# Performance work log

Measured on AMD Instinct MI355X. Metric: run time of the kernel, lower is better.

## Reference

```python
import jax, jax.numpy as jnp
import numpy as np

D_KQ = 1024

def setup_inputs() -> dict:
    key = jax.random.key(0)
    k1, k2, k3, k4, k5 = jax.random.split(key, 5)
    x = jax.random.normal(k1, (4, 2048, 1024), dtype=jnp.float32)
    attention_mask = jax.random.randint(k2, (2048, 2048), 0, 2) == 1
    q_weights = jax.random.normal(k3, (1024, 1024), dtype=jnp.float32)
    k_weights = jax.random.normal(k4, (1024, 1024), dtype=jnp.float32)
    v_weights = jax.random.normal(k5, (1024, 1024), dtype=jnp.float32)
    return {"x": x, "attention_mask": attention_mask,
            "q_weights": q_weights, "k_weights": k_weights, "v_weights": v_weights}

def reference(x, attention_mask, q_weights, k_weights, v_weights):
    # projections: [B,S,d_in] @ [d_in,d] -> [B,S,d]
    query = x @ q_weights
    key = x @ k_weights
    value = x @ v_weights
    # scores: [B,S,S]
    attn_scores = jnp.einsum('bqd,bkd->bqk', query, key)
    masked = jnp.where(attention_mask, -jnp.inf, attn_scores)
    attn_weights = jax.nn.softmax(masked / jnp.sqrt(jnp.float32(D_KQ)), axis=-1)
    return attn_weights @ value
```

## Files before the change

kernel.cpp:

```cpp
#include <hip/hip_runtime.h>
#include <math.h>

static constexpr int BATCH = 4;
static constexpr int SEQ   = 2048;
static constexpr int DIM   = 1024;

typedef __attribute__((ext_vector_type(8))) short     bf16x8;
typedef __attribute__((ext_vector_type(4))) float     f32x4;

__device__ __forceinline__ unsigned short f2b(float v) {
    unsigned int u = __float_as_uint(v);
    u = u + 0x7fffu + ((u >> 16) & 1u);
    return (unsigned short)(u >> 16);
}
__device__ __forceinline__ float b2f(unsigned short h) {
    return __uint_as_float(((unsigned int)h) << 16);
}

__global__ __launch_bounds__(256) void prep_kernel(
    const float* __restrict__ X, const float* __restrict__ Wq,
    const float* __restrict__ Wk, const float* __restrict__ Wv,
    const int* __restrict__ mask,
    unsigned short* __restrict__ Xhi, unsigned short* __restrict__ Xlo,
    unsigned short* __restrict__ Whi, unsigned short* __restrict__ Wlo,
    unsigned short* __restrict__ WvT, unsigned long long* __restrict__ Mb)
{
    __shared__ float t[32][33];
    const int blk = blockIdx.x;
    const int tid = threadIdx.x;

    if (blk < 8192) {
        const int i = blk * 256 + tid;
        const float4 v = ((const float4*)X)[i];
        ushort4 h, l;
        h.x = f2b(v.x); l.x = f2b(v.x - b2f(h.x));
        h.y = f2b(v.y); l.y = f2b(v.y - b2f(h.y));
        h.z = f2b(v.z); l.z = f2b(v.z - b2f(h.z));
        h.w = f2b(v.w); l.w = f2b(v.w - b2f(h.w));
        ((ushort4*)Xhi)[i] = h;
        ((ushort4*)Xlo)[i] = l;
    } else if (blk < 10240) {
        const int lcl = blk - 8192;
        const int z = lcl >> 10;
        const float* __restrict__ W = z ? Wk : Wq;
        const int i = (lcl & 1023) * 256 + tid;
        const int o = z * (DIM * DIM / 4) + i;
        const float4 v = ((const float4*)W)[i];
        ushort4 h, l;
        h.x = f2b(v.x); l.x = f2b(v.x - b2f(h.x));
        h.y = f2b(v.y); l.y = f2b(v.y - b2f(h.y));
        h.z = f2b(v.z); l.z = f2b(v.z - b2f(h.z));
        h.w = f2b(v.w); l.w = f2b(v.w - b2f(h.w));
        ((ushort4*)Whi)[o] = h;
        ((ushort4*)Wlo)[o] = l;
    } else if (blk < 11264) {
        const int lcl = blk - 10240;
        const int n0 = (lcl & 31) * 32, k0 = (lcl >> 5) * 32;
        const int tx = tid & 31, ty = tid >> 5;
#pragma unroll
        for (int i = 0; i < 4; ++i)
            t[ty + i * 8][tx] = Wv[(size_t)(k0 + ty + i * 8) * DIM + (n0 + tx)];
        __syncthreads();
#pragma unroll
        for (int i = 0; i < 4; ++i)
            WvT[(size_t)(n0 + ty + i * 8) * DIM + (k0 + tx)] = f2b(t[tx][ty + i * 8]);
    } else {
        const int row  = blk - 11264;
        const int lane = tid & 63, w = tid >> 6;
#pragma unroll
        for (int c = w; c < SEQ / 64; c += 4) {
            const int v = mask[(size_t)row * SEQ + c * 64 + lane];
            const unsigned long long bits = __ballot(v != 0);
            if (lane == 0) Mb[(size_t)row * (SEQ / 64) + c] = bits;
        }
    }
}

__device__ __forceinline__ void stage_async(
    const unsigned short* __restrict__ g, int gstride, int row0, int k0,
    unsigned short* lds, int tid)
{
    const int w = tid >> 6, lane = tid & 63;
    const int c = (lane & 3) ^ ((lane >> 4) & 3);
#pragma unroll
    for (int h = 0; h < 2; ++h) {
        const int row = 32 * w + 16 * h + (lane >> 2);
        const unsigned short* src = g + (size_t)(row0 + row) * gstride + k0 + 8 * c;
        unsigned short* dst = lds + (32 * w + 16 * h) * 32;
        __builtin_amdgcn_global_load_lds(
            (const __attribute__((address_space(1))) void*)src,
            (__attribute__((address_space(3))) void*)dst, 16, 0, 0);
    }
}

__device__ __forceinline__ void stage128(
    const unsigned short* __restrict__ g, int gstride, int row0, int k0,
    unsigned short* lds, int tid)
{
    const int w = tid >> 6, lane = tid & 63;
    const int c = (lane & 3) ^ ((lane >> 4) & 3);
    const int row = 16 * w + (lane >> 2);
    const unsigned short* src = g + (size_t)(row0 + row) * gstride + k0 + 8 * c;
    unsigned short* dst = lds + (16 * w) * 32;
    __builtin_amdgcn_global_load_lds(
        (const __attribute__((address_space(1))) void*)src,
        (__attribute__((address_space(3))) void*)dst, 16, 0, 0);
}

__device__ __forceinline__ bf16x8 fragr(const unsigned short* lds, int row, int qsw)
{
    return *(const bf16x8*)(lds + row * 32 + qsw * 8);
}

__global__ __launch_bounds__(256) void m_gemm_kernel(
    const unsigned short* __restrict__ Whi, const unsigned short* __restrict__ Wlo,
    float* __restrict__ Mtp)
{
    __shared__ unsigned short Ah[128 * 32], Al[128 * 32];
    __shared__ unsigned short Bh[128 * 32], Bl[128 * 32];

    const int tid = threadIdx.x;
    const int w = tid >> 6, lane = tid & 63;
    const int wm = (w >> 1) * 64, wn = (w & 1) * 64;
    const int m0 = blockIdx.y * 128, n0 = blockIdx.x * 128;
    const int z = blockIdx.z;

    const unsigned short* __restrict__ Ahg = Whi + (size_t)DIM * DIM;
    const unsigned short* __restrict__ Alg = Wlo + (size_t)DIM * DIM;
    const unsigned short* __restrict__ Bhg = Whi;
    const unsigned short* __restrict__ Blg = Wlo;
    float* __restrict__ Cp = Mtp + (size_t)z * DIM * DIM;

    f32x4 acc[4][4];
#pragma unroll
    for (int i = 0; i < 4; ++i)
#pragma unroll
        for (int j = 0; j < 4; ++j) acc[i][j] = (f32x4){0.f, 0.f, 0.f, 0.f};

    const int fr = lane & 15, quad = lane >> 4;
    const int qsw = quad ^ ((fr >> 2) & 3);

    for (int k0 = z * 256; k0 < z * 256 + 256; k0 += 32) {
        stage_async(Ahg, DIM, m0, k0, Ah, tid);
        stage_async(Alg, DIM, m0, k0, Al, tid);
        stage_async(Bhg, DIM, n0, k0, Bh, tid);
        stage_async(Blg, DIM, n0, k0, Bl, tid);
        __syncthreads();

        bf16x8 ah[4], al[4];
#pragma unroll
        for (int mt = 0; mt < 4; ++mt) {
            ah[mt] = fragr(Ah, wm + mt * 16 + fr, qsw);
            al[mt] = fragr(Al, wm + mt * 16 + fr, qsw);
        }
#pragma unroll
        for (int nt = 0; nt < 4; ++nt) {
            const bf16x8 bh = fragr(Bh, wn + nt * 16 + fr, qsw);
            const bf16x8 bl = fragr(Bl, wn + nt * 16 + fr, qsw);
#pragma unroll
            for (int mt = 0; mt < 4; ++mt) {
                acc[mt][nt] = __builtin_amdgcn_mfma_f32_16x16x32_bf16(ah[mt], bh, acc[mt][nt], 0, 0, 0);
                acc[mt][nt] = __builtin_amdgcn_mfma_f32_16x16x32_bf16(ah[mt], bl, acc[mt][nt], 0, 0, 0);
                acc[mt][nt] = __builtin_amdgcn_mfma_f32_16x16x32_bf16(al[mt], bh, acc[mt][nt], 0, 0, 0);
            }
        }
        __syncthreads();
    }

    const int col = lane & 15, rq = lane >> 4;
#pragma unroll
    for (int mt = 0; mt < 4; ++mt)
#pragma unroll
        for (int nt = 0; nt < 4; ++nt)
#pragma unroll
            for (int e = 0; e < 4; ++e) {
                const int m = m0 + wm + mt * 16 + rq * 4 + e;
                const int n = n0 + wn + nt * 16 + col;
                Cp[(size_t)m * DIM + n] = acc[mt][nt][e];
            }
}

__global__ __launch_bounds__(256) void m_reduce_kernel(
    const float* __restrict__ Mtp, unsigned short* __restrict__ Mthi,
    unsigned short* __restrict__ Mtlo)
{
    const int i = blockIdx.x * 256 + threadIdx.x;
    const size_t q = (size_t)DIM * DIM / 4;
    const float4 a = ((const float4*)Mtp)[i];
    const float4 b = ((const float4*)Mtp)[i + q];
    const float4 c = ((const float4*)Mtp)[i + 2 * q];
    const float4 d = ((const float4*)Mtp)[i + 3 * q];
    const float4 v = make_float4(a.x + b.x + c.x + d.x, a.y + b.y + c.y + d.y,
                                 a.z + b.z + c.z + d.z, a.w + b.w + c.w + d.w);
    ushort4 h, l;
    h.x = f2b(v.x); l.x = f2b(v.x - b2f(h.x));
    h.y = f2b(v.y); l.y = f2b(v.y - b2f(h.y));
    h.z = f2b(v.z); l.z = f2b(v.z - b2f(h.z));
    h.w = f2b(v.w); l.w = f2b(v.w - b2f(h.w));
    ((ushort4*)Mthi)[i] = h;
    ((ushort4*)Mtlo)[i] = l;
}

__global__ __launch_bounds__(512, 2) void yv_gemm_kernel(
    const unsigned short* __restrict__ Xhi, const unsigned short* __restrict__ Xlo,
    const unsigned short* __restrict__ Mthi, const unsigned short* __restrict__ Mtlo,
    const unsigned short* __restrict__ WvT,
    unsigned short* __restrict__ Yhi, unsigned short* __restrict__ Ylo,
    unsigned short* __restrict__ Vt)
{
    extern __shared__ unsigned short smem[];

    const int tid = threadIdx.x;
    const int w = tid >> 6, lane = tid & 63;
    const int wm = (w >> 1) * 64, wn = (w & 1) * 64;

    const int flat = blockIdx.x + (blockIdx.y << 3);
    const int xcd = flat & 7, s = flat >> 3;
    const int m0 = (xcd + ((s >> 3) << 3)) * 256;
    const int n0 = (s & 7) * 128;

    f32x4 accY[4][4], accV[4][4];
#pragma unroll
    for (int i = 0; i < 4; ++i)
#pragma unroll
        for (int j = 0; j < 4; ++j) {
            accY[i][j] = (f32x4){0.f, 0.f, 0.f, 0.f};
            accV[i][j] = (f32x4){0.f, 0.f, 0.f, 0.f};
        }

    const int fr = lane & 15, quad = lane >> 4;
    const int qsw = quad ^ ((fr >> 2) & 3);

    stage_async(Xhi, DIM, m0, 0, smem + 0,     tid);
    stage128(Mthi, DIM, n0, 0, smem + 16384, tid);
    stage128(Mtlo, DIM, n0, 0, smem + 20480, tid);
    stage_async(Xlo, DIM, m0, 0, smem + 8192,  tid);
    stage128(WvT,  DIM, n0, 0, smem + 24576, tid);

    bf16x8 ah[4], al[4], bh[4], bl[4], bv[4];

    for (int it = 0; it < DIM / 32 - 1; ++it) {
        const int cur = (it & 1) * 28672;
        const int nxt = 28672 - cur;
        const int k1 = it * 32 + 32;

        stage_async(Xhi, DIM, m0, k1, smem + nxt, tid);
        asm volatile("s_waitcnt vmcnt(6)" ::: "memory");
        __builtin_amdgcn_s_barrier();
#pragma unroll
        for (int mt = 0; mt < 4; ++mt)
            ah[mt] = fragr(smem + cur, wm + mt * 16 + fr, qsw);
#pragma unroll
        for (int nt = 0; nt < 4; ++nt)
            bh[nt] = fragr(smem + cur + 16384, wn + nt * 16 + fr, qsw);
        __builtin_amdgcn_s_setprio(1);
#pragma unroll
        for (int nt = 0; nt < 4; ++nt)
#pragma unroll
            for (int mt = 0; mt < 4; ++mt)
                accY[mt][nt] = __builtin_amdgcn_mfma_f32_16x16x32_bf16(ah[mt], bh[nt], accY[mt][nt], 0, 0, 0);
        __builtin_amdgcn_s_setprio(0);

        stage128(Mthi, DIM, n0, k1, smem + nxt + 16384, tid);
        stage128(Mtlo, DIM, n0, k1, smem + nxt + 20480, tid);
        asm volatile("s_waitcnt vmcnt(7)" ::: "memory");
        __builtin_amdgcn_s_barrier();
#pragma unroll
        for (int nt = 0; nt < 4; ++nt)
            bl[nt] = fragr(smem + cur + 20480, wn + nt * 16 + fr, qsw);
        __builtin_amdgcn_s_setprio(1);
#pragma unroll
        for (int nt = 0; nt < 4; ++nt)
#pragma unroll
            for (int mt = 0; mt < 4; ++mt)
                accY[mt][nt] = __builtin_amdgcn_mfma_f32_16x16x32_bf16(ah[mt], bl[nt], accY[mt][nt], 0, 0, 0);
        __builtin_amdgcn_s_setprio(0);

        stage_async(Xlo, DIM, m0, k1, smem + nxt + 8192, tid);
        asm volatile("s_waitcnt vmcnt(6)" ::: "memory");
        __builtin_amdgcn_s_barrier();
#pragma unroll
        for (int nt = 0; nt < 4; ++nt)
            bv[nt] = fragr(smem + cur + 24576, wn + nt * 16 + fr, qsw);
        __builtin_amdgcn_s_setprio(1);
#pragma unroll
        for (int nt = 0; nt < 4; ++nt)
#pragma unroll
            for (int mt = 0; mt < 4; ++mt)
                accV[mt][nt] = __builtin_amdgcn_mfma_f32_16x16x32_bf16(ah[mt], bv[nt], accV[mt][nt], 0, 0, 0);
        __builtin_amdgcn_s_setprio(0);

        stage128(WvT, DIM, n0, k1, smem + nxt + 24576, tid);
        asm volatile("s_waitcnt vmcnt(8)" ::: "memory");
        __builtin_amdgcn_s_barrier();
#pragma unroll
        for (int mt = 0; mt < 4; ++mt)
            al[mt] = fragr(smem + cur + 8192, wm + mt * 16 + fr, qsw);
        __builtin_amdgcn_s_setprio(1);
#pragma unroll
        for (int nt = 0; nt < 4; ++nt)
#pragma unroll
            for (int mt = 0; mt < 4; ++mt)
                accY[mt][nt] = __builtin_amdgcn_mfma_f32_16x16x32_bf16(al[mt], bh[nt], accY[mt][nt], 0, 0, 0);
        __builtin_amdgcn_s_setprio(0);
    }

    {
        const int cur = 28672;

        asm volatile("s_waitcnt vmcnt(4)" ::: "memory");
        __builtin_amdgcn_s_barrier();
#pragma unroll
        for (int mt = 0; mt < 4; ++mt)
            ah[mt] = fragr(smem + cur, wm + mt * 16 + fr, qsw);
#pragma unroll
        for (int nt = 0; nt < 4; ++nt)
            bh[nt] = fragr(smem + cur + 16384, wn + nt * 16 + fr, qsw);
        __builtin_amdgcn_s_setprio(1);
#pragma unroll
        for (int nt = 0; nt < 4; ++nt)
#pragma unroll
            for (int mt = 0; mt < 4; ++mt)
                accY[mt][nt] = __builtin_amdgcn_mfma_f32_16x16x32_bf16(ah[mt], bh[nt], accY[mt][nt], 0, 0, 0);
        __builtin_amdgcn_s_setprio(0);

        asm volatile("s_waitcnt vmcnt(3)" ::: "memory");
        __builtin_amdgcn_s_barrier();
#pragma unroll
        for (int nt = 0; nt < 4; ++nt)
            bl[nt] = fragr(smem + cur + 20480, wn + nt * 16 + fr, qsw);
        __builtin_amdgcn_s_setprio(1);
#pragma unroll
        for (int nt = 0; nt < 4; ++nt)
#pragma unroll
            for (int mt = 0; mt < 4; ++mt)
                accY[mt][nt] = __builtin_amdgcn_mfma_f32_16x16x32_bf16(ah[mt], bl[nt], accY[mt][nt], 0, 0, 0);
        __builtin_amdgcn_s_setprio(0);

        asm volatile("s_waitcnt vmcnt(0)" ::: "memory");
        __builtin_amdgcn_s_barrier();
#pragma unroll
        for (int nt = 0; nt < 4; ++nt)
            bv[nt] = fragr(smem + cur + 24576, wn + nt * 16 + fr, qsw);
        __builtin_amdgcn_s_setprio(1);
#pragma unroll
        for (int nt = 0; nt < 4; ++nt)
#pragma unroll
            for (int mt = 0; mt < 4; ++mt)
                accV[mt][nt] = __builtin_amdgcn_mfma_f32_16x16x32_bf16(ah[mt], bv[nt], accV[mt][nt], 0, 0, 0);
        __builtin_amdgcn_s_setprio(0);

#pragma unroll
        for (int mt = 0; mt < 4; ++mt)
            al[mt] = fragr(smem + cur + 8192, wm + mt * 16 + fr, qsw);
        __builtin_amdgcn_s_setprio(1);
#pragma unroll
        for (int nt = 0; nt < 4; ++nt)
#pragma unroll
            for (int mt = 0; mt < 4; ++mt)
                accY[mt][nt] = __builtin_amdgcn_mfma_f32_16x16x32_bf16(al[mt], bh[nt], accY[mt][nt], 0, 0, 0);
        __builtin_amdgcn_s_setprio(0);
    }

    const int col = lane & 15, rq = lane >> 4;
#pragma unroll
    for (int mt = 0; mt < 4; ++mt)
#pragma unroll
        for (int nt = 0; nt < 4; ++nt)
#pragma unroll
            for (int e = 0; e < 4; ++e) {
                const int m = m0 + wm + mt * 16 + rq * 4 + e;
                const int n = n0 + wn + nt * 16 + col;
                const float v = accY[mt][nt][e];
                const unsigned short h = f2b(v);
                Yhi[(size_t)m * DIM + n] = h;
                Ylo[(size_t)m * DIM + n] = f2b(v - b2f(h));
            }
#pragma unroll
    for (int mt = 0; mt < 4; ++mt)
#pragma unroll
        for (int nt = 0; nt < 4; ++nt) {
            const int m = m0 + wm + mt * 16 + rq * 4;
            const int bb = m >> 11, sr = m & (SEQ - 1);
            const int n = n0 + wn + nt * 16 + col;
            ushort4 pk;
            pk.x = f2b(accV[mt][nt][0]);
            pk.y = f2b(accV[mt][nt][1]);
            pk.z = f2b(accV[mt][nt][2]);
            pk.w = f2b(accV[mt][nt][3]);
            *(ushort4*)(Vt + (size_t)bb * DIM * SEQ + (size_t)n * SEQ + sr) = pk;
        }
}

__global__ __launch_bounds__(512, 2) void s_gemm256_kernel(
    const unsigned short* __restrict__ Yhi, const unsigned short* __restrict__ Ylo,
    const unsigned short* __restrict__ Xhi, const unsigned short* __restrict__ Xlo,
    const unsigned long long* __restrict__ Mb, float* __restrict__ Sc)
{
    extern __shared__ unsigned short smem[];

    const int tid = threadIdx.x;
    const int w = tid >> 6, lane = tid & 63;
    const int wm = (w >> 2) * 128, wn = (w & 3) * 64;

    const int flat = blockIdx.x + (blockIdx.y << 3) + (blockIdx.z << 6);
    const int lid  = ((flat & 7) << 5) | (flat >> 3);
    const int m0 = ((lid >> 3) & 7) * 256, n0 = (lid & 7) * 256;
    const int b  = lid >> 6;

    const unsigned short* __restrict__ Ahg = Yhi + (size_t)b * SEQ * DIM;
    const unsigned short* __restrict__ Alg = Ylo + (size_t)b * SEQ * DIM;
    const unsigned short* __restrict__ Bhg = Xhi + (size_t)b * SEQ * DIM;
    const unsigned short* __restrict__ Blg = Xlo + (size_t)b * SEQ * DIM;
    float* __restrict__ Sb = Sc + (size_t)b * SEQ * SEQ;

    f32x4 acc[8][4];
#pragma unroll
    for (int i = 0; i < 8; ++i)
#pragma unroll
        for (int j = 0; j < 4; ++j) acc[i][j] = (f32x4){0.f, 0.f, 0.f, 0.f};

    const int fr = lane & 15, quad = lane >> 4;
    const int qsw = quad ^ ((fr >> 2) & 3);

    stage_async(Ahg, DIM, m0, 0, smem + 0,     tid);
    stage_async(Bhg, DIM, n0, 0, smem + 16384, tid);
    stage_async(Blg, DIM, n0, 0, smem + 24576, tid);
    stage_async(Alg, DIM, m0, 0, smem + 8192,  tid);

    for (int it = 0; it < DIM / 32 - 1; ++it) {
        const int cur = (it & 1) * 32768;
        const int nxt = cur ^ 32768;
        const unsigned short* Ah = smem + cur;
        const unsigned short* Al = smem + cur + 8192;
        const unsigned short* Bh = smem + cur + 16384;
        const unsigned short* Bl = smem + cur + 24576;
        const int k1 = it * 32 + 32;

        bf16x8 ah[8], al[8], bh[4], bl[4];

        stage_async(Ahg, DIM, m0, k1, smem + nxt, tid);
        asm volatile("s_waitcnt vmcnt(6)" ::: "memory");
        __builtin_amdgcn_s_barrier();
#pragma unroll
        for (int mt = 0; mt < 4; ++mt)
            ah[mt] = fragr(Ah, wm + mt * 16 + fr, qsw);
#pragma unroll
        for (int nt = 0; nt < 4; ++nt)
            bh[nt] = fragr(Bh, wn + nt * 16 + fr, qsw);
        __builtin_amdgcn_s_setprio(1);
#pragma unroll
        for (int nt = 0; nt < 4; ++nt)
#pragma unroll
            for (int mt = 0; mt < 4; ++mt)
                acc[mt][nt] = __builtin_amdgcn_mfma_f32_16x16x32_bf16(ah[mt], bh[nt], acc[mt][nt], 0, 0, 0);
        __builtin_amdgcn_s_setprio(0);

        stage_async(Bhg, DIM, n0, k1, smem + nxt + 16384, tid);
#pragma unroll
        for (int mt = 4; mt < 8; ++mt)
            ah[mt] = fragr(Ah, wm + mt * 16 + fr, qsw);
        __builtin_amdgcn_s_setprio(1);
#pragma unroll
        for (int nt = 0; nt < 4; ++nt)
#pragma unroll
            for (int mt = 4; mt < 8; ++mt)
                acc[mt][nt] = __builtin_amdgcn_mfma_f32_16x16x32_bf16(ah[mt], bh[nt], acc[mt][nt], 0, 0, 0);
        __builtin_amdgcn_s_setprio(0);

        stage_async(Blg, DIM, n0, k1, smem + nxt + 24576, tid);
        asm volatile("s_waitcnt vmcnt(8)" ::: "memory");
        __builtin_amdgcn_s_barrier();
#pragma unroll
        for (int nt = 0; nt < 4; ++nt)
            bl[nt] = fragr(Bl, wn + nt * 16 + fr, qsw);
        __builtin_amdgcn_s_setprio(1);
#pragma unroll
        for (int nt = 0; nt < 4; ++nt)
#pragma unroll
            for (int mt = 0; mt < 4; ++mt)
                acc[mt][nt] = __builtin_amdgcn_mfma_f32_16x16x32_bf16(ah[mt], bl[nt], acc[mt][nt], 0, 0, 0);
        __builtin_amdgcn_s_setprio(0);

        __builtin_amdgcn_s_setprio(1);
#pragma unroll
        for (int nt = 0; nt < 4; ++nt)
#pragma unroll
            for (int mt = 4; mt < 8; ++mt)
                acc[mt][nt] = __builtin_amdgcn_mfma_f32_16x16x32_bf16(ah[mt], bl[nt], acc[mt][nt], 0, 0, 0);
        __builtin_amdgcn_s_setprio(0);

        stage_async(Alg, DIM, m0, k1, smem + nxt + 8192, tid);
        asm volatile("s_waitcnt vmcnt(8)" ::: "memory");
        __builtin_amdgcn_s_barrier();
#pragma unroll
        for (int mt = 0; mt < 4; ++mt)
            al[mt] = fragr(Al, wm + mt * 16 + fr, qsw);
        __builtin_amdgcn_s_setprio(1);
#pragma unroll
        for (int nt = 0; nt < 4; ++nt)
#pragma unroll
            for (int mt = 0; mt < 4; ++mt)
                acc[mt][nt] = __builtin_amdgcn_mfma_f32_16x16x32_bf16(al[mt], bh[nt], acc[mt][nt], 0, 0, 0);
        __builtin_amdgcn_s_setprio(0);

#pragma unroll
        for (int mt = 4; mt < 8; ++mt)
            al[mt] = fragr(Al, wm + mt * 16 + fr, qsw);
        __builtin_amdgcn_s_setprio(1);
#pragma unroll
        for (int nt = 0; nt < 4; ++nt)
#pragma unroll
            for (int mt = 4; mt < 8; ++mt)
                acc[mt][nt] = __builtin_amdgcn_mfma_f32_16x16x32_bf16(al[mt], bh[nt], acc[mt][nt], 0, 0, 0);
        __builtin_amdgcn_s_setprio(0);
    }

    {
        const unsigned short* Ah = smem + 32768;
        const unsigned short* Al = smem + 32768 + 8192;
        const unsigned short* Bh = smem + 32768 + 16384;
        const unsigned short* Bl = smem + 32768 + 24576;

        bf16x8 ah[8], al[8], bh[4], bl[4];

        asm volatile("s_waitcnt vmcnt(4)" ::: "memory");
        __builtin_amdgcn_s_barrier();
#pragma unroll
        for (int mt = 0; mt < 8; ++mt)
            ah[mt] = fragr(Ah, wm + mt * 16 + fr, qsw);
#pragma unroll
        for (int nt = 0; nt < 4; ++nt)
            bh[nt] = fragr(Bh, wn + nt * 16 + fr, qsw);
        __builtin_amdgcn_s_setprio(1);
#pragma unroll
        for (int nt = 0; nt < 4; ++nt)
#pragma unroll
            for (int mt = 0; mt < 8; ++mt)
                acc[mt][nt] = __builtin_amdgcn_mfma_f32_16x16x32_bf16(ah[mt], bh[nt], acc[mt][nt], 0, 0, 0);
        __builtin_amdgcn_s_setprio(0);

        asm volatile("s_waitcnt vmcnt(2)" ::: "memory");
        __builtin_amdgcn_s_barrier();
#pragma unroll
        for (int nt = 0; nt < 4; ++nt)
            bl[nt] = fragr(Bl, wn + nt * 16 + fr, qsw);
        __builtin_amdgcn_s_setprio(1);
#pragma unroll
        for (int nt = 0; nt < 4; ++nt)
#pragma unroll
            for (int mt = 0; mt < 8; ++mt)
                acc[mt][nt] = __builtin_amdgcn_mfma_f32_16x16x32_bf16(ah[mt], bl[nt], acc[mt][nt], 0, 0, 0);
        __builtin_amdgcn_s_setprio(0);

        asm volatile("s_waitcnt vmcnt(0)" ::: "memory");
        __builtin_amdgcn_s_barrier();
#pragma unroll
        for (int mt = 0; mt < 8; ++mt)
            al[mt] = fragr(Al, wm + mt * 16 + fr, qsw);
        __builtin_amdgcn_s_setprio(1);
#pragma unroll
        for (int nt = 0; nt < 4; ++nt)
#pragma unroll
            for (int mt = 0; mt < 8; ++mt)
                acc[mt][nt] = __builtin_amdgcn_mfma_f32_16x16x32_bf16(al[mt], bh[nt], acc[mt][nt], 0, 0, 0);
        __builtin_amdgcn_s_setprio(0);
    }

    const int col = lane & 15, rq = lane >> 4;
    const int wword = (n0 + wn) >> 6;
#pragma unroll
    for (int mt = 0; mt < 8; ++mt)
#pragma unroll
        for (int e = 0; e < 4; ++e) {
            const int m = m0 + wm + mt * 16 + rq * 4 + e;
            const unsigned long long word = Mb[(size_t)m * (SEQ / 64) + wword];
#pragma unroll
            for (int nt = 0; nt < 4; ++nt) {
                const int n = n0 + wn + nt * 16 + col;
                const float v = acc[mt][nt][e] * 0.03125f;
                const bool msk = (word >> (nt * 16 + col)) & 1ull;
                Sb[(size_t)m * SEQ + n] = msk ? -INFINITY : v;
            }
        }
}

__global__ __launch_bounds__(256) void softmax_kernel(float* __restrict__ Sc)
{
    const int r = blockIdx.x;
    float* __restrict__ row = Sc + (size_t)r * SEQ;

    const int tid  = threadIdx.x;
    const int lane = tid & 63;
    const int wid  = tid >> 6;

    const float4 v0 = ((const float4*)row)[2 * tid];
    const float4 v1 = ((const float4*)row)[2 * tid + 1];
    float x[8] = {v0.x, v0.y, v0.z, v0.w, v1.x, v1.y, v1.z, v1.w};

    float mx = -INFINITY;
#pragma unroll
    for (int j = 0; j < 8; ++j) mx = fmaxf(mx, x[j]);
    __shared__ float redm[4];
#pragma unroll
    for (int off = 32; off > 0; off >>= 1)
        mx = fmaxf(mx, __shfl_down(mx, off, 64));
    if (lane == 0) redm[wid] = mx;
    __syncthreads();
    mx = fmaxf(fmaxf(redm[0], redm[1]), fmaxf(redm[2], redm[3]));

    float sum = 0.f;
#pragma unroll
    for (int j = 0; j < 8; ++j) {
        const float e = __expf(x[j] - mx);
        x[j] = e;
        sum += e;
    }
    __shared__ float reds[4];
#pragma unroll
    for (int off = 32; off > 0; off >>= 1)
        sum += __shfl_down(sum, off, 64);
    if (lane == 0) reds[wid] = sum;
    __syncthreads();
    sum = (reds[0] + reds[1]) + (reds[2] + reds[3]);

    const float inv = 1.0f / sum;
    unsigned short* __restrict__ prow = (unsigned short*)row;
    bf16x8 pk;
#pragma unroll
    for (int j = 0; j < 8; ++j)
        pk[j] = (short)f2b(x[j] * inv);
    *(bf16x8*)(prow + 8 * tid) = pk;
}

__global__ __launch_bounds__(256) void pv_mfma_kernel(
    const unsigned short* __restrict__ P, const unsigned short* __restrict__ Vt,
    float* __restrict__ O)
{
    __shared__ unsigned short As[2][128 * 32], Bs[2][128 * 32];

    const int tid = threadIdx.x;
    const int w = tid >> 6, lane = tid & 63;
    const int wm = (w >> 1) * 64, wn = (w & 1) * 64;

    const int flat = blockIdx.x + (blockIdx.y << 3) + (blockIdx.z << 7);
    const int lid  = ((flat & 7) << 6) | (flat >> 3);
    const int m0 = ((lid >> 3) & 15) * 128, n0 = (lid & 7) * 128;
    const int b  = lid >> 7;

    const unsigned short* __restrict__ Ag = P + (size_t)b * SEQ * (2 * SEQ);
    const unsigned short* __restrict__ Bg = Vt + (size_t)b * DIM * SEQ;
    float* __restrict__ Ob = O + (size_t)b * SEQ * DIM;

    f32x4 acc[4][4];
#pragma unroll
    for (int i = 0; i < 4; ++i)
#pragma unroll
        for (int j = 0; j < 4; ++j) acc[i][j] = (f32x4){0.f, 0.f, 0.f, 0.f};

    const int fr = lane & 15, quad = lane >> 4;
    const int qsw = quad ^ ((fr >> 2) & 3);

    stage_async(Ag, 2 * SEQ, m0, 0, As[0], tid);
    stage_async(Bg, SEQ,     n0, 0, Bs[0], tid);

    for (int it = 0; it < SEQ / 32 - 1; ++it) {
        const int cur = it & 1, nxt = cur ^ 1;
        const int k1 = it * 32 + 32;

        stage_async(Ag, 2 * SEQ, m0, k1, As[nxt], tid);
        stage_async(Bg, SEQ,     n0, k1, Bs[nxt], tid);
        asm volatile("s_waitcnt vmcnt(4)" ::: "memory");
        __builtin_amdgcn_s_barrier();

        bf16x8 af[4];
#pragma unroll
        for (int mt = 0; mt < 4; ++mt)
            af[mt] = fragr(As[cur], wm + mt * 16 + fr, qsw);
        __builtin_amdgcn_s_setprio(1);
#pragma unroll
        for (int nt = 0; nt < 4; ++nt) {
            const bf16x8 bfg = fragr(Bs[cur], wn + nt * 16 + fr, qsw);
#pragma unroll
            for (int mt = 0; mt < 4; ++mt)
                acc[mt][nt] = __builtin_amdgcn_mfma_f32_16x16x32_bf16(af[mt], bfg, acc[mt][nt], 0, 0, 0);
        }
        __builtin_amdgcn_s_setprio(0);
        __builtin_amdgcn_s_barrier();
    }

    {
        asm volatile("s_waitcnt vmcnt(0)" ::: "memory");
        __builtin_amdgcn_s_barrier();
        bf16x8 af[4];
#pragma unroll
        for (int mt = 0; mt < 4; ++mt)
            af[mt] = fragr(As[1], wm + mt * 16 + fr, qsw);
        __builtin_amdgcn_s_setprio(1);
#pragma unroll
        for (int nt = 0; nt < 4; ++nt) {
            const bf16x8 bfg = fragr(Bs[1], wn + nt * 16 + fr, qsw);
#pragma unroll
            for (int mt = 0; mt < 4; ++mt)
                acc[mt][nt] = __builtin_amdgcn_mfma_f32_16x16x32_bf16(af[mt], bfg, acc[mt][nt], 0, 0, 0);
        }
        __builtin_amdgcn_s_setprio(0);
    }

    const int col = lane & 15, rq = lane >> 4;
#pragma unroll
    for (int mt = 0; mt < 4; ++mt)
#pragma unroll
        for (int nt = 0; nt < 4; ++nt)
#pragma unroll
            for (int e = 0; e < 4; ++e) {
                const int m = m0 + wm + mt * 16 + rq * 4 + e;
                const int n = n0 + wn + nt * 16 + col;
                Ob[(size_t)m * DIM + n] = acc[mt][nt][e];
            }
}

extern "C" void kernel_launch(void* const* d_in, const int* in_sizes, int n_in,
                              void* d_out, int out_size, void* d_ws, size_t ws_size,
                              hipStream_t stream)
{
    const float* x    = (const float*)d_in[0];
    const int*   mask = (const int*)d_in[1];
    const float* wq   = (const float*)d_in[2];
    const float* wk   = (const float*)d_in[3];
    const float* wv   = (const float*)d_in[4];
    float* out = (float*)d_out;

    const size_t NQ = (size_t)BATCH * SEQ * DIM;
    const size_t NM = (size_t)DIM * DIM;
    unsigned short* Xhi  = (unsigned short*)d_ws;
    unsigned short* Xlo  = Xhi + NQ;
    unsigned short* Yhi  = Xlo + NQ;
    unsigned short* Ylo  = Yhi + NQ;
    unsigned short* Vt   = Ylo + NQ;
    unsigned short* Mthi = Vt + NQ;
    unsigned short* Mtlo = Mthi + NM;
    float* Sc = (float*)(Mtlo + NM);
    unsigned long long* Mb = (unsigned long long*)(Sc + (size_t)BATCH * SEQ * SEQ);

    unsigned short* Whi = (unsigned short*)Sc;
    unsigned short* Wlo = Whi + 2 * NM;
    unsigned short* WvT = Wlo + 2 * NM;
    float* Mtp = (float*)(WvT + NM);

    static bool lds_attr_set = false;
    if (!lds_attr_set) {
        (void)hipFuncSetAttribute((const void*)s_gemm256_kernel,
                                  hipFuncAttributeMaxDynamicSharedMemorySize,
                                  131072);
        (void)hipFuncSetAttribute((const void*)yv_gemm_kernel,
                                  hipFuncAttributeMaxDynamicSharedMemorySize,
                                  114688);
        lds_attr_set = true;
    }

    prep_kernel<<<dim3(13312), 256, 0, stream>>>(
        x, wq, wk, wv, mask, Xhi, Xlo, Whi, Wlo, WvT, Mb);
    m_gemm_kernel<<<dim3(8, 8, 4), 256, 0, stream>>>(Whi, Wlo, Mtp);
    m_reduce_kernel<<<dim3(NM / 4 / 256), 256, 0, stream>>>(Mtp, Mthi, Mtlo);
    yv_gemm_kernel<<<dim3(DIM / 128, (BATCH * SEQ) / 256), 512, 114688, stream>>>(
        Xhi, Xlo, Mthi, Mtlo, WvT, Yhi, Ylo, Vt);
    s_gemm256_kernel<<<dim3(SEQ / 256, SEQ / 256, BATCH), 512, 131072, stream>>>(
        Yhi, Ylo, Xhi, Xlo, Mb, Sc);
    softmax_kernel<<<dim3(BATCH * SEQ), 256, 0, stream>>>(Sc);
    pv_mfma_kernel<<<dim3(DIM / 128, SEQ / 128, BATCH), 256, 0, stream>>>(
        (const unsigned short*)Sc, Vt, out);
}
```

Baseline: 341.2 us.

## Fuse segment max and exp into score GEMM epilogue, store bf16 exps

The score GEMM epilogue now computes a per-64-column segment max through a 16-lane shuffle reduction, applies exp against that local max, and stores bf16 exponentials plus the segment maxima. It no longer writes fp32 scores. The softmax kernel then only reads the 32 segment maxima, rescales the bf16 values, and normalizes in place. This halves score traffic and removes the max pass from softmax. The cost is extra exp and shuffle work in the GEMM epilogue, and a loss of precision because exponentials are rounded to bf16 before rescaling.

```diff
diff --git a/kernel.cpp b/kernel.cpp
--- a/kernel.cpp
+++ b/kernel.cpp
@@ -395,7 +395,8 @@
 __global__ __launch_bounds__(512, 2) void s_gemm256_kernel(
     const unsigned short* __restrict__ Yhi, const unsigned short* __restrict__ Ylo,
     const unsigned short* __restrict__ Xhi, const unsigned short* __restrict__ Xlo,
-    const unsigned long long* __restrict__ Mb, float* __restrict__ Sc)
+    const unsigned long long* __restrict__ Mb, float* __restrict__ Sc,
+    float* __restrict__ Mx)
 {
     extern __shared__ unsigned short smem[];
 
@@ -412,7 +413,9 @@
     const unsigned short* __restrict__ Alg = Ylo + (size_t)b * SEQ * DIM;
     const unsigned short* __restrict__ Bhg = Xhi + (size_t)b * SEQ * DIM;
     const unsigned short* __restrict__ Blg = Xlo + (size_t)b * SEQ * DIM;
-    float* __restrict__ Sb = Sc + (size_t)b * SEQ * SEQ;
+    unsigned short* __restrict__ Eb =
+        (unsigned short*)(Sc + (size_t)b * SEQ * SEQ);
+    float* __restrict__ MxB = Mx + (size_t)b * SEQ * (SEQ / 64);
 
     f32x4 acc[8][4];
 #pragma unroll
@@ -575,47 +578,56 @@
         for (int e = 0; e < 4; ++e) {
             const int m = m0 + wm + mt * 16 + rq * 4 + e;
             const unsigned long long word = Mb[(size_t)m * (SEQ / 64) + wword];
+            float sv[4];
+            float mx = -INFINITY;
+#pragma unroll
+            for (int nt = 0; nt < 4; ++nt) {
+                const bool msk = (word >> (nt * 16 + col)) & 1ull;
+                sv[nt] = msk ? -INFINITY : acc[mt][nt][e] * 0.03125f;
+                mx = fmaxf(mx, sv[nt]);
+            }
+#pragma unroll
+            for (int off = 1; off < 16; off <<= 1)
+                mx = fmaxf(mx, __shfl_xor(mx, off, 16));
 #pragma unroll
             for (int nt = 0; nt < 4; ++nt) {
                 const int n = n0 + wn + nt * 16 + col;
-                const float v = acc[mt][nt][e] * 0.03125f;
-                const bool msk = (word >> (nt * 16 + col)) & 1ull;
-                Sb[(size_t)m * SEQ + n] = msk ? -INFINITY : v;
+                const float ev = (sv[nt] == -INFINITY) ? 0.f : __expf(sv[nt] - mx);
+                Eb[(size_t)m * (2 * SEQ) + n] = f2b(ev);
             }
+            if (col == 0)
+                MxB[(size_t)m * (SEQ / 64) + wword] = mx;
         }
 }
 
-__global__ __launch_bounds__(256) void softmax_kernel(float* __restrict__ Sc)
+__global__ __launch_bounds__(256) void softmax_kernel(
+    float* __restrict__ Sc, const float* __restrict__ Mx)
 {
     const int r = blockIdx.x;
-    float* __restrict__ row = Sc + (size_t)r * SEQ;
+    unsigned short* __restrict__ prow = (unsigned short*)(Sc + (size_t)r * SEQ);
 
     const int tid  = threadIdx.x;
     const int lane = tid & 63;
     const int wid  = tid >> 6;
 
-    const float4 v0 = ((const float4*)row)[2 * tid];
-    const float4 v1 = ((const float4*)row)[2 * tid + 1];
-    float x[8] = {v0.x, v0.y, v0.z, v0.w, v1.x, v1.y, v1.z, v1.w};
-
-    float mx = -INFINITY;
-#pragma unroll
-    for (int j = 0; j < 8; ++j) mx = fmaxf(mx, x[j]);
-    __shared__ float redm[4];
-#pragma unroll
-    for (int off = 32; off > 0; off >>= 1)
-        mx = fmaxf(mx, __shfl_down(mx, off, 64));
-    if (lane == 0) redm[wid] = mx;
+    __shared__ float seg[32];
+    if (tid < 32) seg[tid] = Mx[(size_t)r * 32 + tid];
     __syncthreads();
-    mx = fmaxf(fmaxf(redm[0], redm[1]), fmaxf(redm[2], redm[3]));
-
-    float sum = 0.f;
+    float M = -INFINITY;
+#pragma unroll
+    for (int j = 0; j < 32; ++j) M = fmaxf(M, seg[j]);
+
+    const float f = __expf(seg[tid >> 3] - M);
+
+    const bf16x8 ev = *(const bf16x8*)(prow + 8 * tid);
+    float x[8];
+    float psum = 0.f;
 #pragma unroll
     for (int j = 0; j < 8; ++j) {
-        const float e = __expf(x[j] - mx);
-        x[j] = e;
-        sum += e;
-    }
+        x[j] = b2f((unsigned short)ev[j]);
+        psum += x[j];
+    }
+    float sum = psum * f;
     __shared__ float reds[4];
 #pragma unroll
     for (int off = 32; off > 0; off >>= 1)
@@ -624,12 +636,11 @@
     __syncthreads();
     sum = (reds[0] + reds[1]) + (reds[2] + reds[3]);
 
-    const float inv = 1.0f / sum;
-    unsigned short* __restrict__ prow = (unsigned short*)row;
+    const float fi = f / sum;
     bf16x8 pk;
 #pragma unroll
     for (int j = 0; j < 8; ++j)
-        pk[j] = (short)f2b(x[j] * inv);
+        pk[j] = (short)f2b(x[j] * fi);
     *(bf16x8*)(prow + 8 * tid) = pk;
 }
 
@@ -742,6 +753,7 @@
     unsigned short* Mtlo = Mthi + NM;
     float* Sc = (float*)(Mtlo + NM);
     unsigned long long* Mb = (unsigned long long*)(Sc + (size_t)BATCH * SEQ * SEQ);
+    float* Mx = (float*)(Mb + (size_t)SEQ * (SEQ / 64));
 
     unsigned short* Whi = (unsigned short*)Sc;
     unsigned short* Wlo = Whi + 2 * NM;
@@ -766,8 +778,8 @@
     yv_gemm_kernel<<<dim3(DIM / 128, (BATCH * SEQ) / 256), 512, 114688, stream>>>(
         Xhi, Xlo, Mthi, Mtlo, WvT, Yhi, Ylo, Vt);
     s_gemm256_kernel<<<dim3(SEQ / 256, SEQ / 256, BATCH), 512, 131072, stream>>>(
-        Yhi, Ylo, Xhi, Xlo, Mb, Sc);
-    softmax_kernel<<<dim3(BATCH * SEQ), 256, 0, stream>>>(Sc);
+        Yhi, Ylo, Xhi, Xlo, Mb, Sc, Mx);
+    softmax_kernel<<<dim3(BATCH * SEQ), 256, 0, stream>>>(Sc, Mx);
     pv_mfma_kernel<<<dim3(DIM / 128, SEQ / 128, BATCH), 256, 0, stream>>>(
         (const unsigned short*)Sc, Vt, out);
 }
```

After: 352.7 us. 1.03x slower.
